# Optimization experiments

Hardware: AMD Instinct MI355X
Metric: run time of the kernel (lower is better)

Reference implementation:

```python
import jax, jax.numpy as jnp
import numpy as np

T = 20.0
SCALE = 0.3


def setup_inputs() -> dict:
    key = jax.random.key(0)
    k1, k2, k3 = jax.random.split(key, 3)
    N, C = 65536, 1000
    outputs1 = jax.random.normal(k1, (N, C), dtype=jnp.float32)
    outputs2 = jax.random.normal(k2, (N, C), dtype=jnp.float32)
    targets = jax.random.randint(k3, (N,), 0, C, dtype=jnp.int64)
    return {"outputs1": outputs1, "outputs2": outputs2, "targets": targets}


def reference(outputs1, outputs2, targets):
    # temperature softmax over classes
    p1 = jax.nn.softmax(outputs1 / T, axis=1)  # [N, C]
    p2 = jax.nn.softmax(outputs2 / T, axis=1)  # [N, C]
    # mean-center each row
    vx = p1 - jnp.mean(p1, axis=1, keepdims=True)
    vy = p2 - jnp.mean(p2, axis=1, keepdims=True)
    # per-row Pearson correlation
    num = jnp.sum(vx * vy, axis=1)
    den = jnp.sqrt(jnp.sum(vx * vx, axis=1)) * jnp.sqrt(jnp.sum(vy * vy, axis=1))
    cost = num / den  # [N]
    return jnp.mean(SCALE * cost)
```

## Files before the change

kernel.cpp:

```cpp
#include <hip/hip_runtime.h>


#define N_ROWS  65536
#define N_C     1000
#define NBLOCKS 2048
#define WPB     4
#define RPW     8
#define RSTEP   (NBLOCKS * WPB)

__device__ __forceinline__ const float4* rp(const float* o, int row) {
    return reinterpret_cast<const float4*>(o + (long)row * N_C);
}

__device__ __forceinline__ void accum_row(
        float4 a0, float4 a1, float4 a2, float4 a3,
        float4 b0, float4 b1, float4 b2, float4 b3,
        bool tail_ok, double& acc) {
    constexpr float INV_T = 1.0f / 20.0f;
    float sx = 0.f, sy = 0.f, sxx = 0.f, syy = 0.f, sxy = 0.f;
    float va[16] = {a0.x, a0.y, a0.z, a0.w, a1.x, a1.y, a1.z, a1.w,
                    a2.x, a2.y, a2.z, a2.w, a3.x, a3.y, a3.z, a3.w};
    float vb[16] = {b0.x, b0.y, b0.z, b0.w, b1.x, b1.y, b1.z, b1.w,
                    b2.x, b2.y, b2.z, b2.w, b3.x, b3.y, b3.z, b3.w};
    #pragma unroll
    for (int e = 0; e < 16; ++e) {
        const bool ok = (e < 12) || tail_ok;
        float fa = ok ? va[e] : 0.0f;
        float fb = ok ? vb[e] : 0.0f;
        float x = __expf(fa * INV_T) - 1.0f;
        float y = __expf(fb * INV_T) - 1.0f;
        sx += x;  sy += y;
        sxx = fmaf(x, x, sxx);
        syy = fmaf(y, y, syy);
        sxy = fmaf(x, y, sxy);
    }
    #pragma unroll
    for (int off = 32; off; off >>= 1) {
        sx  += __shfl_xor(sx,  off, 64);
        sy  += __shfl_xor(sy,  off, 64);
        sxx += __shfl_xor(sxx, off, 64);
        syy += __shfl_xor(syy, off, 64);
        sxy += __shfl_xor(sxy, off, 64);
    }
    constexpr double invC = 1.0 / (double)N_C;
    double dx = (double)sx, dy = (double)sy;
    double num = (double)sxy - dx * dy * invC;
    double vx  = (double)sxx - dx * dx * invC;
    double vy  = (double)syy - dy * dy * invC;
    acc += num / sqrt(vx * vy);
}

__global__ __launch_bounds__(256) void div2_stage1(
        const float* __restrict__ o1, const float* __restrict__ o2,
        double* __restrict__ ws) {
    const int wave = threadIdx.x >> 6;
    const int lane = threadIdx.x & 63;
    const int gw   = blockIdx.x * WPB + wave;
    const int i3   = (lane < 58) ? (192 + lane) : 0;
    const bool tail_ok = (lane < 58);

    int r = gw;
    double acc = 0.0;

    const float4* A = rp(o1, r);
    const float4* B = rp(o2, r);
    float4 pa0 = A[lane], pa1 = A[64 + lane], pa2 = A[128 + lane], pa3 = A[i3];
    float4 pb0 = B[lane], pb1 = B[64 + lane], pb2 = B[128 + lane], pb3 = B[i3];

    #pragma unroll 1
    for (int p = 0; p < RPW - 2; p += 2) {
        const float4* A1 = rp(o1, r + RSTEP);
        const float4* B1 = rp(o2, r + RSTEP);
        float4 qa0 = A1[lane], qa1 = A1[64 + lane], qa2 = A1[128 + lane], qa3 = A1[i3];
        float4 qb0 = B1[lane], qb1 = B1[64 + lane], qb2 = B1[128 + lane], qb3 = B1[i3];
        accum_row(pa0, pa1, pa2, pa3, pb0, pb1, pb2, pb3, tail_ok, acc);

        const float4* A2 = rp(o1, r + 2 * RSTEP);
        const float4* B2 = rp(o2, r + 2 * RSTEP);
        pa0 = A2[lane]; pa1 = A2[64 + lane]; pa2 = A2[128 + lane]; pa3 = A2[i3];
        pb0 = B2[lane]; pb1 = B2[64 + lane]; pb2 = B2[128 + lane]; pb3 = B2[i3];
        accum_row(qa0, qa1, qa2, qa3, qb0, qb1, qb2, qb3, tail_ok, acc);

        r += 2 * RSTEP;
    }

    {
        const float4* A1 = rp(o1, r + RSTEP);
        const float4* B1 = rp(o2, r + RSTEP);
        float4 qa0 = A1[lane], qa1 = A1[64 + lane], qa2 = A1[128 + lane], qa3 = A1[i3];
        float4 qb0 = B1[lane], qb1 = B1[64 + lane], qb2 = B1[128 + lane], qb3 = B1[i3];
        accum_row(pa0, pa1, pa2, pa3, pb0, pb1, pb2, pb3, tail_ok, acc);
        accum_row(qa0, qa1, qa2, qa3, qb0, qb1, qb2, qb3, tail_ok, acc);
    }

    __shared__ double dred[WPB];
    if (lane == 0) dred[wave] = acc;
    __syncthreads();
    if (threadIdx.x == 0)
        ws[blockIdx.x] = dred[0] + dred[1] + dred[2] + dred[3];
}

__global__ __launch_bounds__(256) void div2_stage2(
        const double* __restrict__ ws, int n, float* __restrict__ out) {
    double s = 0.0;
    for (int i = threadIdx.x; i < n; i += 256) s += ws[i];
    #pragma unroll
    for (int off = 32; off; off >>= 1) s += __shfl_xor(s, off, 64);
    __shared__ double lds[4];
    const int wave = threadIdx.x >> 6;
    const int lane = threadIdx.x & 63;
    if (lane == 0) lds[wave] = s;
    __syncthreads();
    if (threadIdx.x == 0) {
        double t = lds[0] + lds[1] + lds[2] + lds[3];
        out[0] = (float)(t * (0.3 / (double)N_ROWS));
    }
}

extern "C" void kernel_launch(void* const* d_in, const int* in_sizes, int n_in,
                              void* d_out, int out_size, void* d_ws, size_t ws_size,
                              hipStream_t stream) {
    const float* o1 = (const float*)d_in[0];
    const float* o2 = (const float*)d_in[1];
    float* out = (float*)d_out;
    double* ws = (double*)d_ws;

    div2_stage1<<<NBLOCKS, 256, 0, stream>>>(o1, o2, ws);
    div2_stage2<<<1, 256, 0, stream>>>(ws, NBLOCKS, out);
}
```

Measured before the change: 96.09 us.

## Launch one block per two rows per wave instead of software-pipelined loop

```diff
diff --git a/kernel.cpp b/kernel.cpp
--- a/kernel.cpp
+++ b/kernel.cpp
@@ -3,10 +3,7 @@
 
 #define N_ROWS  65536
 #define N_C     1000
-#define NBLOCKS 2048
 #define WPB     4
-#define RPW     8
-#define RSTEP   (NBLOCKS * WPB)
 
 __device__ __forceinline__ const float4* rp(const float* o, int row) {
     return reinterpret_cast<const float4*>(o + (long)row * N_C);
@@ -52,41 +49,25 @@
 
 __global__ __launch_bounds__(256) void div2_stage1(
         const float* __restrict__ o1, const float* __restrict__ o2,
-        double* __restrict__ ws) {
-    const int wave = threadIdx.x >> 6;
-    const int lane = threadIdx.x & 63;
-    const int gw   = blockIdx.x * WPB + wave;
-    const int i3   = (lane < 58) ? (192 + lane) : 0;
+        double* __restrict__ ws, int batches) {
+    const int wave   = threadIdx.x >> 6;
+    const int lane   = threadIdx.x & 63;
+    const int nwaves = gridDim.x * WPB;
+    const int gw     = blockIdx.x * WPB + wave;
+    const int i3     = (lane < 58) ? (192 + lane) : 0;
     const bool tail_ok = (lane < 58);
 
-    int r = gw;
     double acc = 0.0;
-
-    const float4* A = rp(o1, r);
-    const float4* B = rp(o2, r);
-    float4 pa0 = A[lane], pa1 = A[64 + lane], pa2 = A[128 + lane], pa3 = A[i3];
-    float4 pb0 = B[lane], pb1 = B[64 + lane], pb2 = B[128 + lane], pb3 = B[i3];
-
     #pragma unroll 1
-    for (int p = 0; p < RPW - 2; p += 2) {
-        const float4* A1 = rp(o1, r + RSTEP);
-        const float4* B1 = rp(o2, r + RSTEP);
-        float4 qa0 = A1[lane], qa1 = A1[64 + lane], qa2 = A1[128 + lane], qa3 = A1[i3];
-        float4 qb0 = B1[lane], qb1 = B1[64 + lane], qb2 = B1[128 + lane], qb3 = B1[i3];
-        accum_row(pa0, pa1, pa2, pa3, pb0, pb1, pb2, pb3, tail_ok, acc);
-
-        const float4* A2 = rp(o1, r + 2 * RSTEP);
-        const float4* B2 = rp(o2, r + 2 * RSTEP);
-        pa0 = A2[lane]; pa1 = A2[64 + lane]; pa2 = A2[128 + lane]; pa3 = A2[i3];
-        pb0 = B2[lane]; pb1 = B2[64 + lane]; pb2 = B2[128 + lane]; pb3 = B2[i3];
-        accum_row(qa0, qa1, qa2, qa3, qb0, qb1, qb2, qb3, tail_ok, acc);
-
-        r += 2 * RSTEP;
-    }
-
-    {
-        const float4* A1 = rp(o1, r + RSTEP);
-        const float4* B1 = rp(o2, r + RSTEP);
+    for (int b = 0; b < batches; ++b) {
+        const int r0 = gw + b * 2 * nwaves;
+        const int r1 = r0 + nwaves;
+        const float4* A0 = rp(o1, r0);
+        const float4* B0 = rp(o2, r0);
+        const float4* A1 = rp(o1, r1);
+        const float4* B1 = rp(o2, r1);
+        float4 pa0 = A0[lane], pa1 = A0[64 + lane], pa2 = A0[128 + lane], pa3 = A0[i3];
+        float4 pb0 = B0[lane], pb1 = B0[64 + lane], pb2 = B0[128 + lane], pb3 = B0[i3];
         float4 qa0 = A1[lane], qa1 = A1[64 + lane], qa2 = A1[128 + lane], qa3 = A1[i3];
         float4 qb0 = B1[lane], qb1 = B1[64 + lane], qb2 = B1[128 + lane], qb3 = B1[i3];
         accum_row(pa0, pa1, pa2, pa3, pb0, pb1, pb2, pb3, tail_ok, acc);
@@ -125,6 +106,9 @@
     float* out = (float*)d_out;
     double* ws = (double*)d_ws;
 
-    div2_stage1<<<NBLOCKS, 256, 0, stream>>>(o1, o2, ws);
-    div2_stage2<<<1, 256, 0, stream>>>(ws, NBLOCKS, out);
+    int nblocks = 8192, batches = 1;
+    if (ws_size < (size_t)nblocks * sizeof(double)) { nblocks = 2048; batches = 4; }
+
+    div2_stage1<<<nblocks, 256, 0, stream>>>(o1, o2, ws, batches);
+    div2_stage2<<<1, 256, 0, stream>>>(ws, nblocks, out);
 }
```

After: 103.9 us. 1.08x slower.
